# Kernel optimization log

Hardware: AMD Instinct MI355X
Metric: run time of the kernel (lower is better)

## Reference

```python
import jax, jax.numpy as jnp
import numpy as np

N_NODES = 50000
N_EDGES = 1600000
IN_CH = 128
HID = 64
HEADS = 2
EMB = 128
OUT_CH = EMB // HEADS  # 64, GATConvMean out_channels
NEG_SLOPE = 0.2


def _gat_conv(x, src, dst, W, a_src, a_dst, b, heads, out_ch, concat, n_nodes):
    # x: [N, F_in]; W: [F_in, heads*out_ch]; a_src/a_dst: [heads, out_ch]; b: bias
    s = (x @ W).reshape(n_nodes, heads, out_ch)          # [N, H, C]
    alpha_src = jnp.sum(s * a_src, axis=-1)              # [N, H]
    alpha_dst = jnp.sum(s * a_dst, axis=-1)              # [N, H]
    e = jax.nn.leaky_relu(alpha_src[src] + alpha_dst[dst], NEG_SLOPE)  # [E, H]
    # segment softmax over edges sharing the same destination node
    m = jax.ops.segment_max(e, dst, num_segments=n_nodes)             # [N, H]
    ex = jnp.exp(e - m[dst])
    denom = jax.ops.segment_sum(ex, dst, num_segments=n_nodes)        # [N, H]
    alpha = ex / denom[dst]                                           # [E, H]
    msg = s[src] * alpha[:, :, None]                                  # [E, H, C]
    out = jax.ops.segment_sum(msg, dst, num_segments=n_nodes)         # [N, H, C]
    if concat:
        out = out.reshape(n_nodes, heads * out_ch)
    else:
        out = out.mean(axis=1)
    return out + b


def setup_inputs() -> dict:
    key = jax.random.key(0)
    ks = jax.random.split(key, 16)
    X = jax.random.normal(ks[0], (N_NODES, IN_CH), dtype=jnp.float32)
    edge_index = jax.random.randint(ks[1], (2, N_EDGES), 0, N_NODES, dtype=jnp.int64)

    def glorot(k, shape):
        fan_in, fan_out = shape[0], shape[-1]
        lim = jnp.sqrt(6.0 / (fan_in + fan_out)).astype(jnp.float32)
        return jax.random.uniform(k, shape, jnp.float32, -lim, lim)

    HC = HEADS * HID  # 128
    # in_layer: GATConv(IN_CH -> HID, heads=HEADS, concat)
    W0 = glorot(ks[2], (IN_CH, HC))
    a_src0 = glorot(ks[3], (HEADS, HID))
    a_dst0 = glorot(ks[4], (HEADS, HID))
    b0 = jnp.zeros((HC,), jnp.float32)
    # middle layer: GATConv(HC -> HID, heads=HEADS, concat)
    W1 = glorot(ks[5], (HC, HC))
    a_src1 = glorot(ks[6], (HEADS, HID))
    a_dst1 = glorot(ks[7], (HEADS, HID))
    b1 = jnp.zeros((HC,), jnp.float32)
    # ivectors: GATConvMean(HC -> OUT_CH, heads=HEADS, mean over heads)
    W2 = glorot(ks[8], (HC, HEADS * OUT_CH))
    a_src2 = glorot(ks[9], (HEADS, OUT_CH))
    a_dst2 = glorot(ks[10], (HEADS, OUT_CH))
    b2 = jnp.zeros((OUT_CH,), jnp.float32)
    return {
        "X": X, "edge_index": edge_index,
        "W0": W0, "a_src0": a_src0, "a_dst0": a_dst0, "b0": b0,
        "W1": W1, "a_src1": a_src1, "a_dst1": a_dst1, "b1": b1,
        "W2": W2, "a_src2": a_src2, "a_dst2": a_dst2, "b2": b2,
    }


def reference(X, edge_index, W0, a_src0, a_dst0, b0, W1, a_src1, a_dst1, b1, W2, a_src2, a_dst2, b2):
    n = X.shape[0]
    loop = jnp.arange(n, dtype=edge_index.dtype)
    src = jnp.concatenate([edge_index[0], loop])  # PyG GATConv add_self_loops=True
    dst = jnp.concatenate([edge_index[1], loop])
    h = jax.nn.elu(_gat_conv(X, src, dst, W0, a_src0, a_dst0, b0, HEADS, HID, True, n))
    h = jax.nn.relu(_gat_conv(h, src, dst, W1, a_src1, a_dst1, b1, HEADS, HID, True, n))
    # dropout is identity in eval mode
    out = jax.nn.relu(_gat_conv(h, src, dst, W2, a_src2, a_dst2, b2, HEADS, OUT_CH, False, n))
    return out
```

## Files before the change

kernel.cpp:

```cpp
#include <hip/hip_runtime.h>
#include <hip/hip_bf16.h>


#define SCAN_BLOCK 256

__global__ void detect_i64(const unsigned* __restrict__ ei, int* __restrict__ flag) {
    if (threadIdx.x == 0 && blockIdx.x == 0) {
        int allz = 1;
        for (int i = 0; i < 128; ++i)
            if (ei[2 * i + 1] != 0u) { allz = 0; break; }
        *flag = allz;
    }
}

__global__ __launch_bounds__(256) void gat_rank(
    const void* __restrict__ ei, const int* __restrict__ flag, int nE, int nN,
    int* __restrict__ cnt, int* __restrict__ rank) {
    const int i64 = *flag;
    const int cw = (nN + 7) >> 3;
    const int lo = (blockIdx.x & 7) * cw;
    const long long total = (long long)nE + nN;
    const long long stride = (long long)(gridDim.x >> 3) * blockDim.x;
    for (long long i = (long long)(blockIdx.x >> 3) * blockDim.x + threadIdx.x;
         i < total; i += stride) {
        int d;
        if (i < nE) d = i64 ? (int)((const long long*)ei)[nE + i] : ((const int*)ei)[nE + i];
        else        d = (int)(i - nE);
        if ((unsigned)(d - lo) >= (unsigned)cw) continue;
        rank[i] = atomicAdd(&cnt[d], 1);
    }
}

__global__ __launch_bounds__(SCAN_BLOCK) void scan_stage1(
    const int* __restrict__ cnt, int* __restrict__ partial, int* __restrict__ bsum, int n) {
    __shared__ int tmp[SCAN_BLOCK];
    const int i = blockIdx.x * SCAN_BLOCK + threadIdx.x;
    const int v = (i < n) ? cnt[i] : 0;
    tmp[threadIdx.x] = v;
    __syncthreads();
    #pragma unroll
    for (int off = 1; off < SCAN_BLOCK; off <<= 1) {
        const int t = (threadIdx.x >= off) ? tmp[threadIdx.x - off] : 0;
        __syncthreads();
        tmp[threadIdx.x] += t;
        __syncthreads();
    }
    if (i < n) partial[i] = tmp[threadIdx.x];
    if (threadIdx.x == SCAN_BLOCK - 1) bsum[blockIdx.x] = tmp[threadIdx.x];
}

__global__ void scan_stage2(int* __restrict__ bsum, int nb, int* __restrict__ rowp, int n) {
    const int lane = threadIdx.x;
    int carry = 0;
    for (int base = 0; base < nb; base += 64) {
        const int i = base + lane;
        const int v = (i < nb) ? bsum[i] : 0;
        int incl = v;
        #pragma unroll
        for (int off = 1; off < 64; off <<= 1) {
            const int t = __shfl_up(incl, off);
            if (lane >= off) incl += t;
        }
        if (i < nb) bsum[i] = carry + incl - v;
        carry += __shfl(incl, 63);
    }
    if (lane == 0) rowp[n] = carry;
}

__global__ __launch_bounds__(SCAN_BLOCK) void scan_stage3(
    const int* __restrict__ partial, const int* __restrict__ cnt, const int* __restrict__ bsum,
    int* __restrict__ rowp, int n) {
    const int i = blockIdx.x * SCAN_BLOCK + threadIdx.x;
    if (i < n) rowp[i] = bsum[i >> 8] + partial[i] - cnt[i];
}

__global__ __launch_bounds__(256) void gat_place(
    const void* __restrict__ ei, const int* __restrict__ flag, int nE, int nN,
    const int* __restrict__ rowp, const int* __restrict__ rank, int* __restrict__ csr) {
    const int i64 = *flag;
    const int cw = (nN + 7) >> 3;
    const int lo = (blockIdx.x & 7) * cw;
    const long long total = (long long)nE + nN;
    const long long stride = (long long)(gridDim.x >> 3) * blockDim.x;
    for (long long i = (long long)(blockIdx.x >> 3) * blockDim.x + threadIdx.x;
         i < total; i += stride) {
        int s, d;
        if (i < nE) {
            d = i64 ? (int)((const long long*)ei)[nE + i] : ((const int*)ei)[nE + i];
            if ((unsigned)(d - lo) >= (unsigned)cw) continue;
            s = i64 ? (int)((const long long*)ei)[i] : ((const int*)ei)[i];
        } else {
            s = d = (int)(i - nE);
            if ((unsigned)(d - lo) >= (unsigned)cw) continue;
        }
        csr[rowp[d] + rank[i]] = s;
    }
}

__global__ __launch_bounds__(256) void gemm_alpha(
    const float* __restrict__ Xin, const float* __restrict__ W,
    const float* __restrict__ avs, const float* __restrict__ avd,
    float* __restrict__ S, float* __restrict__ as_, float* __restrict__ ad_, int n) {
    __shared__ float Xl[64][128];
    const int tid = threadIdx.x;
    const int row0 = blockIdx.x * 64;
    for (int i = tid; i < 64 * 32; i += 256) {
        const int r = i >> 5, c4 = i & 31;
        const int gr = row0 + r;
        float4 v = (gr < n) ? ((const float4*)(Xin + (size_t)gr * 128))[c4]
                            : make_float4(0.f, 0.f, 0.f, 0.f);
        ((float4*)(&Xl[r][0]))[c4] = v;
    }
    __syncthreads();
    const int col4 = tid & 31;
    const int rowg = tid >> 5;
    float4 acc[8];
    #pragma unroll
    for (int r = 0; r < 8; ++r) acc[r] = make_float4(0.f, 0.f, 0.f, 0.f);
    const float* Wc = W + col4 * 4;
    for (int kk = 0; kk < 128; kk += 4) {
        const float4 w0 = *(const float4*)(Wc + (size_t)(kk + 0) * 128);
        const float4 w1 = *(const float4*)(Wc + (size_t)(kk + 1) * 128);
        const float4 w2 = *(const float4*)(Wc + (size_t)(kk + 2) * 128);
        const float4 w3 = *(const float4*)(Wc + (size_t)(kk + 3) * 128);
        #pragma unroll
        for (int r = 0; r < 8; ++r) {
            const float4 x = *(const float4*)(&Xl[rowg * 8 + r][kk]);
            acc[r].x = fmaf(x.x, w0.x, acc[r].x); acc[r].y = fmaf(x.x, w0.y, acc[r].y);
            acc[r].z = fmaf(x.x, w0.z, acc[r].z); acc[r].w = fmaf(x.x, w0.w, acc[r].w);
            acc[r].x = fmaf(x.y, w1.x, acc[r].x); acc[r].y = fmaf(x.y, w1.y, acc[r].y);
            acc[r].z = fmaf(x.y, w1.z, acc[r].z); acc[r].w = fmaf(x.y, w1.w, acc[r].w);
            acc[r].x = fmaf(x.z, w2.x, acc[r].x); acc[r].y = fmaf(x.z, w2.y, acc[r].y);
            acc[r].z = fmaf(x.z, w2.z, acc[r].z); acc[r].w = fmaf(x.z, w2.w, acc[r].w);
            acc[r].x = fmaf(x.w, w3.x, acc[r].x); acc[r].y = fmaf(x.w, w3.y, acc[r].y);
            acc[r].z = fmaf(x.w, w3.z, acc[r].z); acc[r].w = fmaf(x.w, w3.w, acc[r].w);
        }
    }
    const float4 av = ((const float4*)avs)[col4];
    const float4 dv = ((const float4*)avd)[col4];
    #pragma unroll
    for (int r = 0; r < 8; ++r) {
        const int grow = row0 + rowg * 8 + r;
        if (grow < n) ((float4*)(S + (size_t)grow * 128))[col4] = acc[r];
        float ps = acc[r].x * av.x + acc[r].y * av.y + acc[r].z * av.z + acc[r].w * av.w;
        float pd = acc[r].x * dv.x + acc[r].y * dv.y + acc[r].z * dv.z + acc[r].w * dv.w;
        #pragma unroll
        for (int off = 8; off; off >>= 1) {
            ps += __shfl_xor(ps, off);
            pd += __shfl_xor(pd, off);
        }
        if ((col4 & 15) == 0 && grow < n) {
            const int h = col4 >> 4;
            as_[2 * grow + h] = ps;
            ad_[2 * grow + h] = pd;
        }
    }
}

__global__ __launch_bounds__(256) void gat_stats(
    const float* __restrict__ as_, const float* __restrict__ ad_,
    const int* __restrict__ rowp, const int* __restrict__ csr,
    float2* __restrict__ alpha, int n) {
    const int lane = threadIdx.x & 63;
    const int d = (blockIdx.x * blockDim.x + threadIdx.x) >> 6;
    if (d >= n) return;
    const int beg = rowp[d], end = rowp[d + 1];
    const float2 adv = *(const float2*)(ad_ + 2 * d);
    if (end - beg <= 64) {
        const int i = beg + lane;
        const bool has = i < end;
        float e0 = -1e30f, e1 = -1e30f;
        if (has) {
            const int s = csr[i];
            const float2 asv = *(const float2*)(as_ + 2 * s);
            e0 = asv.x + adv.x; e0 = e0 > 0.f ? e0 : 0.2f * e0;
            e1 = asv.y + adv.y; e1 = e1 > 0.f ? e1 : 0.2f * e1;
        }
        float m0 = e0, m1 = e1;
        #pragma unroll
        for (int off = 32; off; off >>= 1) {
            m0 = fmaxf(m0, __shfl_xor(m0, off));
            m1 = fmaxf(m1, __shfl_xor(m1, off));
        }
        float p0 = has ? __expf(e0 - m0) : 0.f;
        float p1 = has ? __expf(e1 - m1) : 0.f;
        float s0 = p0, s1 = p1;
        #pragma unroll
        for (int off = 32; off; off >>= 1) {
            s0 += __shfl_xor(s0, off);
            s1 += __shfl_xor(s1, off);
        }
        if (has) alpha[i] = make_float2(p0 / s0, p1 / s1);
    } else {
        float m0 = -1e30f, m1 = -1e30f;
        for (int i = beg + lane; i < end; i += 64) {
            const int s = csr[i];
            const float2 asv = *(const float2*)(as_ + 2 * s);
            float e0 = asv.x + adv.x; e0 = e0 > 0.f ? e0 : 0.2f * e0;
            float e1 = asv.y + adv.y; e1 = e1 > 0.f ? e1 : 0.2f * e1;
            m0 = fmaxf(m0, e0); m1 = fmaxf(m1, e1);
        }
        #pragma unroll
        for (int off = 32; off; off >>= 1) {
            m0 = fmaxf(m0, __shfl_xor(m0, off));
            m1 = fmaxf(m1, __shfl_xor(m1, off));
        }
        float s0 = 0.f, s1 = 0.f;
        for (int i = beg + lane; i < end; i += 64) {
            const int s = csr[i];
            const float2 asv = *(const float2*)(as_ + 2 * s);
            float e0 = asv.x + adv.x; e0 = e0 > 0.f ? e0 : 0.2f * e0;
            float e1 = asv.y + adv.y; e1 = e1 > 0.f ? e1 : 0.2f * e1;
            s0 += __expf(e0 - m0); s1 += __expf(e1 - m1);
        }
        #pragma unroll
        for (int off = 32; off; off >>= 1) {
            s0 += __shfl_xor(s0, off);
            s1 += __shfl_xor(s1, off);
        }
        const float r0 = 1.f / s0, r1 = 1.f / s1;
        for (int i = beg + lane; i < end; i += 64) {
            const int s = csr[i];
            const float2 asv = *(const float2*)(as_ + 2 * s);
            float e0 = asv.x + adv.x; e0 = e0 > 0.f ? e0 : 0.2f * e0;
            float e1 = asv.y + adv.y; e1 = e1 > 0.f ? e1 : 0.2f * e1;
            alpha[i] = make_float2(__expf(e0 - m0) * r0, __expf(e1 - m1) * r1);
        }
    }
}

__global__ __launch_bounds__(256) void gat_gather(
    const float* __restrict__ S, const float2* __restrict__ alpha,
    const int* __restrict__ rowp, const int* __restrict__ csr,
    const float* __restrict__ bias, float* __restrict__ out, int n, int mode) {
    const int lane = threadIdx.x & 63;
    const int d = (blockIdx.x * blockDim.x + threadIdx.x) >> 6;
    if (d >= n) return;
    const int beg = rowp[d], end = rowp[d + 1];
    const int g  = lane >> 4;
    const int gl = lane & 15;
    float4 acc0 = make_float4(0.f, 0.f, 0.f, 0.f);
    float4 acc1 = make_float4(0.f, 0.f, 0.f, 0.f);
    int i = beg;
    for (; i + 8 <= end; i += 8) {
        const int j0 = i + g, j1 = i + 4 + g;
        const int sa = csr[j0], sb = csr[j1];
        const float2 aa = alpha[j0], ab = alpha[j1];
        const float4* ra = (const float4*)(S + ((size_t)sa << 7));
        const float4* rb = (const float4*)(S + ((size_t)sb << 7));
        const float4 va0 = ra[gl], va1 = ra[16 + gl];
        const float4 vb0 = rb[gl], vb1 = rb[16 + gl];
        acc0.x = fmaf(aa.x, va0.x, acc0.x); acc0.y = fmaf(aa.x, va0.y, acc0.y);
        acc0.z = fmaf(aa.x, va0.z, acc0.z); acc0.w = fmaf(aa.x, va0.w, acc0.w);
        acc1.x = fmaf(aa.y, va1.x, acc1.x); acc1.y = fmaf(aa.y, va1.y, acc1.y);
        acc1.z = fmaf(aa.y, va1.z, acc1.z); acc1.w = fmaf(aa.y, va1.w, acc1.w);
        acc0.x = fmaf(ab.x, vb0.x, acc0.x); acc0.y = fmaf(ab.x, vb0.y, acc0.y);
        acc0.z = fmaf(ab.x, vb0.z, acc0.z); acc0.w = fmaf(ab.x, vb0.w, acc0.w);
        acc1.x = fmaf(ab.y, vb1.x, acc1.x); acc1.y = fmaf(ab.y, vb1.y, acc1.y);
        acc1.z = fmaf(ab.y, vb1.z, acc1.z); acc1.w = fmaf(ab.y, vb1.w, acc1.w);
    }
    for (; i < end; i += 4) {
        const int j = i + g;
        const bool valid = j < end;
        const int jj = valid ? j : beg;
        const int s = csr[jj];
        const float2 a2 = alpha[jj];
        const float a0 = valid ? a2.x : 0.f;
        const float a1 = valid ? a2.y : 0.f;
        const float4* r = (const float4*)(S + ((size_t)s << 7));
        const float4 v0 = r[gl], v1 = r[16 + gl];
        acc0.x = fmaf(a0, v0.x, acc0.x); acc0.y = fmaf(a0, v0.y, acc0.y);
        acc0.z = fmaf(a0, v0.z, acc0.z); acc0.w = fmaf(a0, v0.w, acc0.w);
        acc1.x = fmaf(a1, v1.x, acc1.x); acc1.y = fmaf(a1, v1.y, acc1.y);
        acc1.z = fmaf(a1, v1.z, acc1.z); acc1.w = fmaf(a1, v1.w, acc1.w);
    }
    #pragma unroll
    for (int off = 16; off <= 32; off <<= 1) {
        acc0.x += __shfl_xor(acc0.x, off); acc0.y += __shfl_xor(acc0.y, off);
        acc0.z += __shfl_xor(acc0.z, off); acc0.w += __shfl_xor(acc0.w, off);
        acc1.x += __shfl_xor(acc1.x, off); acc1.y += __shfl_xor(acc1.y, off);
        acc1.z += __shfl_xor(acc1.z, off); acc1.w += __shfl_xor(acc1.w, off);
    }
    if (mode == 2) {
        if (lane < 16) {
            const float4 b = ((const float4*)bias)[gl];
            float4 o;
            o.x = fmaxf(0.5f * (acc0.x + acc1.x) + b.x, 0.f);
            o.y = fmaxf(0.5f * (acc0.y + acc1.y) + b.y, 0.f);
            o.z = fmaxf(0.5f * (acc0.z + acc1.z) + b.z, 0.f);
            o.w = fmaxf(0.5f * (acc0.w + acc1.w) + b.w, 0.f);
            ((float4*)(out + (size_t)d * 64))[gl] = o;
        }
    } else if (lane < 32) {
        const int ci = (lane < 16) ? gl : 16 + gl;
        const float4 a = (lane < 16) ? acc0 : acc1;
        const float4 b = ((const float4*)bias)[ci];
        float4 o;
        o.x = a.x + b.x; o.y = a.y + b.y; o.z = a.z + b.z; o.w = a.w + b.w;
        if (mode == 0) {
            o.x = o.x > 0.f ? o.x : expm1f(o.x);
            o.y = o.y > 0.f ? o.y : expm1f(o.y);
            o.z = o.z > 0.f ? o.z : expm1f(o.z);
            o.w = o.w > 0.f ? o.w : expm1f(o.w);
        } else {
            o.x = fmaxf(o.x, 0.f); o.y = fmaxf(o.y, 0.f);
            o.z = fmaxf(o.z, 0.f); o.w = fmaxf(o.w, 0.f);
        }
        ((float4*)(out + (size_t)d * 128))[ci] = o;
    }
}

extern "C" void kernel_launch(void* const* d_in, const int* in_sizes, int n_in,
                              void* d_out, int out_size, void* d_ws, size_t ws_size,
                              hipStream_t stream) {
    const float* X   = (const float*)d_in[0];
    const void*  EI  = d_in[1];
    const float* W0  = (const float*)d_in[2];
    const float* as0 = (const float*)d_in[3];
    const float* ad0 = (const float*)d_in[4];
    const float* b0  = (const float*)d_in[5];
    const float* W1  = (const float*)d_in[6];
    const float* as1 = (const float*)d_in[7];
    const float* ad1 = (const float*)d_in[8];
    const float* b1  = (const float*)d_in[9];
    const float* W2  = (const float*)d_in[10];
    const float* as2 = (const float*)d_in[11];
    const float* ad2 = (const float*)d_in[12];
    const float* b2  = (const float*)d_in[13];

    const int N  = in_sizes[0] / 128;
    const int E  = in_sizes[1] / 2;
    const int ET = E + N;
    const int NB = (N + SCAN_BLOCK - 1) / SCAN_BLOCK;

    char* p = (char*)d_ws;
    size_t used = 0;
    auto alloc = [&](size_t bytes) -> void* {
        void* r = p + used;
        used += (bytes + 255) & ~(size_t)255;
        return r;
    };
    float*  S    = (float*)alloc((size_t)N * 128 * 4);
    float*  H0   = (float*)alloc((size_t)N * 128 * 4);
    float*  H1   = (float*)alloc((size_t)N * 128 * 4);
    int*    csr  = (int*)alloc((size_t)ET * 4);
    float2* alp  = (float2*)alloc((size_t)ET * 8);
    int*    rowp = (int*)alloc((size_t)(N + 1) * 4);
    int*    cnt  = (int*)alloc((size_t)N * 4);
    int*    part = (int*)alloc((size_t)N * 4);
    int*    bsum = (int*)alloc((size_t)NB * 4);
    float*  asb  = (float*)alloc((size_t)N * 2 * 4);
    float*  adb  = (float*)alloc((size_t)N * 2 * 4);
    int*    flag = (int*)alloc(256);
    if (used > ws_size) return;
    int* rank = (int*)alp;

    hipMemsetAsync(cnt, 0, (size_t)N * 4, stream);
    detect_i64<<<1, 64, 0, stream>>>((const unsigned*)EI, flag);
    gat_rank<<<2048, 256, 0, stream>>>(EI, flag, E, N, cnt, rank);
    scan_stage1<<<NB, SCAN_BLOCK, 0, stream>>>(cnt, part, bsum, N);
    scan_stage2<<<1, 64, 0, stream>>>(bsum, NB, rowp, N);
    scan_stage3<<<NB, SCAN_BLOCK, 0, stream>>>(part, cnt, bsum, rowp, N);
    gat_place<<<2048, 256, 0, stream>>>(EI, flag, E, N, rowp, rank, csr);

    const int gemm_blocks = (N + 63) / 64;
    const int wave_blocks = (N + 3) / 4;

    gemm_alpha<<<gemm_blocks, 256, 0, stream>>>(X, W0, as0, ad0, S, asb, adb, N);
    gat_stats<<<wave_blocks, 256, 0, stream>>>(asb, adb, rowp, csr, alp, N);
    gat_gather<<<wave_blocks, 256, 0, stream>>>(S, alp, rowp, csr, b0, H0, N, 0);
    gemm_alpha<<<gemm_blocks, 256, 0, stream>>>(H0, W1, as1, ad1, S, asb, adb, N);
    gat_stats<<<wave_blocks, 256, 0, stream>>>(asb, adb, rowp, csr, alp, N);
    gat_gather<<<wave_blocks, 256, 0, stream>>>(S, alp, rowp, csr, b1, H1, N, 1);
    gemm_alpha<<<gemm_blocks, 256, 0, stream>>>(H1, W2, as2, ad2, S, asb, adb, N);
    gat_stats<<<wave_blocks, 256, 0, stream>>>(asb, adb, rowp, csr, alp, N);
    gat_gather<<<wave_blocks, 256, 0, stream>>>(S, alp, rowp, csr, b2, (float*)d_out, N, 2);
}
```

Measured before the change: 588.8 us.

## Fuse softmax stats into gather kernel and stage unpacked edge indices for CSR build

Merges the per-layer attention softmax kernel and the aggregation kernel into one wave-per-node kernel. The source index and softmax weights stay in registers and are broadcast with shuffles, so the alpha array is no longer written and re-read. Separately, the CSR rank pass now runs without destination partitioning and writes unpacked int32 src/dst arrays into the S buffer, which the place pass reads instead of the int64 edge list. This drops three launches and an edge-sized round trip per layer. In exchange the gather loses its 8-edge unroll, and the rank atomics lose the locality the partitioning gave them.

```diff
diff --git a/kernel.cpp b/kernel.cpp
--- a/kernel.cpp
+++ b/kernel.cpp
@@ -15,18 +15,19 @@
 
 __global__ __launch_bounds__(256) void gat_rank(
     const void* __restrict__ ei, const int* __restrict__ flag, int nE, int nN,
-    int* __restrict__ cnt, int* __restrict__ rank) {
+    int* __restrict__ cnt, int* __restrict__ rank,
+    int* __restrict__ srci, int* __restrict__ dsti) {
     const int i64 = *flag;
-    const int cw = (nN + 7) >> 3;
-    const int lo = (blockIdx.x & 7) * cw;
     const long long total = (long long)nE + nN;
-    const long long stride = (long long)(gridDim.x >> 3) * blockDim.x;
-    for (long long i = (long long)(blockIdx.x >> 3) * blockDim.x + threadIdx.x;
-         i < total; i += stride) {
-        int d;
-        if (i < nE) d = i64 ? (int)((const long long*)ei)[nE + i] : ((const int*)ei)[nE + i];
-        else        d = (int)(i - nE);
-        if ((unsigned)(d - lo) >= (unsigned)cw) continue;
+    const long long stride = (long long)gridDim.x * blockDim.x;
+    for (long long i = (long long)blockIdx.x * blockDim.x + threadIdx.x; i < total; i += stride) {
+        int s, d;
+        if (i < nE) {
+            if (i64) { s = (int)((const long long*)ei)[i]; d = (int)((const long long*)ei)[nE + i]; }
+            else     { s = ((const int*)ei)[i];            d = ((const int*)ei)[nE + i]; }
+        } else { s = d = (int)(i - nE); }
+        srci[i] = s;
+        dsti[i] = d;
         rank[i] = atomicAdd(&cnt[d], 1);
     }
 }
@@ -75,25 +76,17 @@
 }
 
 __global__ __launch_bounds__(256) void gat_place(
-    const void* __restrict__ ei, const int* __restrict__ flag, int nE, int nN,
-    const int* __restrict__ rowp, const int* __restrict__ rank, int* __restrict__ csr) {
-    const int i64 = *flag;
+    const int* __restrict__ srci, const int* __restrict__ dsti,
+    const int* __restrict__ rank, const int* __restrict__ rowp,
+    long long total, int nN, int* __restrict__ csr) {
     const int cw = (nN + 7) >> 3;
     const int lo = (blockIdx.x & 7) * cw;
-    const long long total = (long long)nE + nN;
     const long long stride = (long long)(gridDim.x >> 3) * blockDim.x;
     for (long long i = (long long)(blockIdx.x >> 3) * blockDim.x + threadIdx.x;
          i < total; i += stride) {
-        int s, d;
-        if (i < nE) {
-            d = i64 ? (int)((const long long*)ei)[nE + i] : ((const int*)ei)[nE + i];
-            if ((unsigned)(d - lo) >= (unsigned)cw) continue;
-            s = i64 ? (int)((const long long*)ei)[i] : ((const int*)ei)[i];
-        } else {
-            s = d = (int)(i - nE);
-            if ((unsigned)(d - lo) >= (unsigned)cw) continue;
-        }
-        csr[rowp[d] + rank[i]] = s;
+        const int d = dsti[i];
+        if ((unsigned)(d - lo) >= (unsigned)cw) continue;
+        csr[rowp[d] + rank[i]] = srci[i];
     }
 }
 
@@ -157,22 +150,27 @@
     }
 }
 
-__global__ __launch_bounds__(256) void gat_stats(
-    const float* __restrict__ as_, const float* __restrict__ ad_,
-    const int* __restrict__ rowp, const int* __restrict__ csr,
-    float2* __restrict__ alpha, int n) {
+__global__ __launch_bounds__(256) void gat_fused(
+    const float* __restrict__ S, const float* __restrict__ as_,
+    const float* __restrict__ ad_, const int* __restrict__ rowp,
+    const int* __restrict__ csr, const float* __restrict__ bias,
+    float* __restrict__ out, int n, int mode) {
     const int lane = threadIdx.x & 63;
     const int d = (blockIdx.x * blockDim.x + threadIdx.x) >> 6;
     if (d >= n) return;
     const int beg = rowp[d], end = rowp[d + 1];
+    const int deg = end - beg;
     const float2 adv = *(const float2*)(ad_ + 2 * d);
-    if (end - beg <= 64) {
-        const int i = beg + lane;
-        const bool has = i < end;
+    const int g = lane >> 4;
+    const int gl = lane & 15;
+    float4 acc0 = make_float4(0.f, 0.f, 0.f, 0.f);
+    float4 acc1 = make_float4(0.f, 0.f, 0.f, 0.f);
+    if (deg <= 64) {
+        const bool has = lane < deg;
+        const int s_reg = has ? csr[beg + lane] : 0;
         float e0 = -1e30f, e1 = -1e30f;
         if (has) {
-            const int s = csr[i];
-            const float2 asv = *(const float2*)(as_ + 2 * s);
+            const float2 asv = *(const float2*)(as_ + 2 * s_reg);
             e0 = asv.x + adv.x; e0 = e0 > 0.f ? e0 : 0.2f * e0;
             e1 = asv.y + adv.y; e1 = e1 > 0.f ? e1 : 0.2f * e1;
         }
@@ -182,15 +180,43 @@
             m0 = fmaxf(m0, __shfl_xor(m0, off));
             m1 = fmaxf(m1, __shfl_xor(m1, off));
         }
-        float p0 = has ? __expf(e0 - m0) : 0.f;
-        float p1 = has ? __expf(e1 - m1) : 0.f;
+        const float p0 = has ? __expf(e0 - m0) : 0.f;
+        const float p1 = has ? __expf(e1 - m1) : 0.f;
         float s0 = p0, s1 = p1;
         #pragma unroll
         for (int off = 32; off; off >>= 1) {
             s0 += __shfl_xor(s0, off);
             s1 += __shfl_xor(s1, off);
         }
-        if (has) alpha[i] = make_float2(p0 / s0, p1 / s1);
+        const float inv0 = 1.f / s0, inv1 = 1.f / s1;
+        int k = 0;
+        for (; k + 4 <= deg; k += 4) {
+            const int ke = k + g;
+            const int sv = __shfl(s_reg, ke);
+            const float a0 = __shfl(p0, ke) * inv0;
+            const float a1 = __shfl(p1, ke) * inv1;
+            const float4* r = (const float4*)(S + ((size_t)sv << 7));
+            const float4 v0 = r[gl], v1 = r[16 + gl];
+            acc0.x = fmaf(a0, v0.x, acc0.x); acc0.y = fmaf(a0, v0.y, acc0.y);
+            acc0.z = fmaf(a0, v0.z, acc0.z); acc0.w = fmaf(a0, v0.w, acc0.w);
+            acc1.x = fmaf(a1, v1.x, acc1.x); acc1.y = fmaf(a1, v1.y, acc1.y);
+            acc1.z = fmaf(a1, v1.z, acc1.z); acc1.w = fmaf(a1, v1.w, acc1.w);
+        }
+        if (k < deg) {
+            const int ke = k + g;
+            const bool valid = ke < deg;
+            const int idx = valid ? ke : 0;
+            const int sv = __shfl(s_reg, idx);
+            const float q0 = __shfl(p0, idx), q1 = __shfl(p1, idx);
+            const float a0 = valid ? q0 * inv0 : 0.f;
+            const float a1 = valid ? q1 * inv1 : 0.f;
+            const float4* r = (const float4*)(S + ((size_t)sv << 7));
+            const float4 v0 = r[gl], v1 = r[16 + gl];
+            acc0.x = fmaf(a0, v0.x, acc0.x); acc0.y = fmaf(a0, v0.y, acc0.y);
+            acc0.z = fmaf(a0, v0.z, acc0.z); acc0.w = fmaf(a0, v0.w, acc0.w);
+            acc1.x = fmaf(a1, v1.x, acc1.x); acc1.y = fmaf(a1, v1.y, acc1.y);
+            acc1.z = fmaf(a1, v1.z, acc1.z); acc1.w = fmaf(a1, v1.w, acc1.w);
+        }
     } else {
         float m0 = -1e30f, m1 = -1e30f;
         for (int i = beg + lane; i < end; i += 64) {
@@ -218,61 +244,24 @@
             s0 += __shfl_xor(s0, off);
             s1 += __shfl_xor(s1, off);
         }
-        const float r0 = 1.f / s0, r1 = 1.f / s1;
-        for (int i = beg + lane; i < end; i += 64) {
-            const int s = csr[i];
-            const float2 asv = *(const float2*)(as_ + 2 * s);
+        const float inv0 = 1.f / s0, inv1 = 1.f / s1;
+        for (int k = 0; k < deg; k += 4) {
+            const int ke = k + g;
+            const bool valid = ke < deg;
+            const int j = beg + (valid ? ke : 0);
+            const int sv = csr[j];
+            const float2 asv = *(const float2*)(as_ + 2 * sv);
             float e0 = asv.x + adv.x; e0 = e0 > 0.f ? e0 : 0.2f * e0;
             float e1 = asv.y + adv.y; e1 = e1 > 0.f ? e1 : 0.2f * e1;
-            alpha[i] = make_float2(__expf(e0 - m0) * r0, __expf(e1 - m1) * r1);
-        }
-    }
-}
-
-__global__ __launch_bounds__(256) void gat_gather(
-    const float* __restrict__ S, const float2* __restrict__ alpha,
-    const int* __restrict__ rowp, const int* __restrict__ csr,
-    const float* __restrict__ bias, float* __restrict__ out, int n, int mode) {
-    const int lane = threadIdx.x & 63;
-    const int d = (blockIdx.x * blockDim.x + threadIdx.x) >> 6;
-    if (d >= n) return;
-    const int beg = rowp[d], end = rowp[d + 1];
-    const int g  = lane >> 4;
-    const int gl = lane & 15;
-    float4 acc0 = make_float4(0.f, 0.f, 0.f, 0.f);
-    float4 acc1 = make_float4(0.f, 0.f, 0.f, 0.f);
-    int i = beg;
-    for (; i + 8 <= end; i += 8) {
-        const int j0 = i + g, j1 = i + 4 + g;
-        const int sa = csr[j0], sb = csr[j1];
-        const float2 aa = alpha[j0], ab = alpha[j1];
-        const float4* ra = (const float4*)(S + ((size_t)sa << 7));
-        const float4* rb = (const float4*)(S + ((size_t)sb << 7));
-        const float4 va0 = ra[gl], va1 = ra[16 + gl];
-        const float4 vb0 = rb[gl], vb1 = rb[16 + gl];
-        acc0.x = fmaf(aa.x, va0.x, acc0.x); acc0.y = fmaf(aa.x, va0.y, acc0.y);
-        acc0.z = fmaf(aa.x, va0.z, acc0.z); acc0.w = fmaf(aa.x, va0.w, acc0.w);
-        acc1.x = fmaf(aa.y, va1.x, acc1.x); acc1.y = fmaf(aa.y, va1.y, acc1.y);
-        acc1.z = fmaf(aa.y, va1.z, acc1.z); acc1.w = fmaf(aa.y, va1.w, acc1.w);
-        acc0.x = fmaf(ab.x, vb0.x, acc0.x); acc0.y = fmaf(ab.x, vb0.y, acc0.y);
-        acc0.z = fmaf(ab.x, vb0.z, acc0.z); acc0.w = fmaf(ab.x, vb0.w, acc0.w);
-        acc1.x = fmaf(ab.y, vb1.x, acc1.x); acc1.y = fmaf(ab.y, vb1.y, acc1.y);
-        acc1.z = fmaf(ab.y, vb1.z, acc1.z); acc1.w = fmaf(ab.y, vb1.w, acc1.w);
-    }
-    for (; i < end; i += 4) {
-        const int j = i + g;
-        const bool valid = j < end;
-        const int jj = valid ? j : beg;
-        const int s = csr[jj];
-        const float2 a2 = alpha[jj];
-        const float a0 = valid ? a2.x : 0.f;
-        const float a1 = valid ? a2.y : 0.f;
-        const float4* r = (const float4*)(S + ((size_t)s << 7));
-        const float4 v0 = r[gl], v1 = r[16 + gl];
-        acc0.x = fmaf(a0, v0.x, acc0.x); acc0.y = fmaf(a0, v0.y, acc0.y);
-        acc0.z = fmaf(a0, v0.z, acc0.z); acc0.w = fmaf(a0, v0.w, acc0.w);
-        acc1.x = fmaf(a1, v1.x, acc1.x); acc1.y = fmaf(a1, v1.y, acc1.y);
-        acc1.z = fmaf(a1, v1.z, acc1.z); acc1.w = fmaf(a1, v1.w, acc1.w);
+            const float a0 = valid ? __expf(e0 - m0) * inv0 : 0.f;
+            const float a1 = valid ? __expf(e1 - m1) * inv1 : 0.f;
+            const float4* r = (const float4*)(S + ((size_t)sv << 7));
+            const float4 v0 = r[gl], v1 = r[16 + gl];
+            acc0.x = fmaf(a0, v0.x, acc0.x); acc0.y = fmaf(a0, v0.y, acc0.y);
+            acc0.z = fmaf(a0, v0.z, acc0.z); acc0.w = fmaf(a0, v0.w, acc0.w);
+            acc1.x = fmaf(a1, v1.x, acc1.x); acc1.y = fmaf(a1, v1.y, acc1.y);
+            acc1.z = fmaf(a1, v1.z, acc1.z); acc1.w = fmaf(a1, v1.w, acc1.w);
+        }
     }
     #pragma unroll
     for (int off = 16; off <= 32; off <<= 1) {
@@ -344,7 +333,6 @@
     float*  H0   = (float*)alloc((size_t)N * 128 * 4);
     float*  H1   = (float*)alloc((size_t)N * 128 * 4);
     int*    csr  = (int*)alloc((size_t)ET * 4);
-    float2* alp  = (float2*)alloc((size_t)ET * 8);
     int*    rowp = (int*)alloc((size_t)(N + 1) * 4);
     int*    cnt  = (int*)alloc((size_t)N * 4);
     int*    part = (int*)alloc((size_t)N * 4);
@@ -353,26 +341,26 @@
     float*  adb  = (float*)alloc((size_t)N * 2 * 4);
     int*    flag = (int*)alloc(256);
     if (used > ws_size) return;
-    int* rank = (int*)alp;
+    const int ETP = (ET + 63) & ~63;
+    int* srci = (int*)S;
+    int* dsti = srci + ETP;
+    int* rank = dsti + ETP;
 
     hipMemsetAsync(cnt, 0, (size_t)N * 4, stream);
     detect_i64<<<1, 64, 0, stream>>>((const unsigned*)EI, flag);
-    gat_rank<<<2048, 256, 0, stream>>>(EI, flag, E, N, cnt, rank);
+    gat_rank<<<2048, 256, 0, stream>>>(EI, flag, E, N, cnt, rank, srci, dsti);
     scan_stage1<<<NB, SCAN_BLOCK, 0, stream>>>(cnt, part, bsum, N);
     scan_stage2<<<1, 64, 0, stream>>>(bsum, NB, rowp, N);
     scan_stage3<<<NB, SCAN_BLOCK, 0, stream>>>(part, cnt, bsum, rowp, N);
-    gat_place<<<2048, 256, 0, stream>>>(EI, flag, E, N, rowp, rank, csr);
+    gat_place<<<2048, 256, 0, stream>>>(srci, dsti, rank, rowp, (long long)ET, N, csr);
 
     const int gemm_blocks = (N + 63) / 64;
     const int wave_blocks = (N + 3) / 4;
 
     gemm_alpha<<<gemm_blocks, 256, 0, stream>>>(X, W0, as0, ad0, S, asb, adb, N);
-    gat_stats<<<wave_blocks, 256, 0, stream>>>(asb, adb, rowp, csr, alp, N);
-    gat_gather<<<wave_blocks, 256, 0, stream>>>(S, alp, rowp, csr, b0, H0, N, 0);
+    gat_fused<<<wave_blocks, 256, 0, stream>>>(S, asb, adb, rowp, csr, b0, H0, N, 0);
     gemm_alpha<<<gemm_blocks, 256, 0, stream>>>(H0, W1, as1, ad1, S, asb, adb, N);
-    gat_stats<<<wave_blocks, 256, 0, stream>>>(asb, adb, rowp, csr, alp, N);
-    gat_gather<<<wave_blocks, 256, 0, stream>>>(S, alp, rowp, csr, b1, H1, N, 1);
+    gat_fused<<<wave_blocks, 256, 0, stream>>>(S, asb, adb, rowp, csr, b1, H1, N, 1);
     gemm_alpha<<<gemm_blocks, 256, 0, stream>>>(H1, W2, as2, ad2, S, asb, adb, N);
-    gat_stats<<<wave_blocks, 256, 0, stream>>>(asb, adb, rowp, csr, alp, N);
-    gat_gather<<<wave_blocks, 256, 0, stream>>>(S, alp, rowp, csr, b2, (float*)d_out, N, 2);
-}
+    gat_fused<<<wave_blocks, 256, 0, stream>>>(S, asb, adb, rowp, csr, b2, (float*)d_out, N, 2);
+}
```

Measured after the change: 579.8 us. Within noise of the previous version (-1.5%).
